# Performance work log

Hardware: AMD Instinct MI355X
Metric: run time of the kernel (lower is better)

Reference implementation:

```python
import jax, jax.numpy as jnp
import numpy as np

N = 50000      # nodes
E = 800000     # edges
F = 128        # input features
H = 128        # hidden dim
G = 1024       # graphs in batch
EPS = 1e-5


def setup_inputs() -> dict:
    key = jax.random.key(0)
    ks = jax.random.split(key, 16)
    s = 0.05
    return {
        "x": jax.random.normal(ks[0], (N, F), dtype=jnp.float32),
        "edge_index": jax.random.randint(ks[1], (2, E), 0, N, dtype=jnp.int64),
        "batch": jnp.sort(jax.random.randint(ks[2], (N,), 0, G, dtype=jnp.int64)),
        "convW0": jax.random.normal(ks[3], (F, H), dtype=jnp.float32) * s,
        "convW": jax.random.normal(ks[4], (2, H, H), dtype=jnp.float32) * s,  # layers 1,2
        "convb": jax.random.normal(ks[5], (3, H), dtype=jnp.float32) * s,
        "bn_gamma": jnp.ones((3, H), dtype=jnp.float32),
        "bn_beta": jnp.zeros((3, H), dtype=jnp.float32),
        "mW1": jax.random.normal(ks[6], (2 * H, 256), dtype=jnp.float32) * s,
        "mb1": jnp.zeros((256,), dtype=jnp.float32),
        "mW2": jax.random.normal(ks[7], (256, 128), dtype=jnp.float32) * s,
        "mb2": jnp.zeros((128,), dtype=jnp.float32),
        "mW3": jax.random.normal(ks[8], (128, 1), dtype=jnp.float32) * s,
        "mb3": jnp.zeros((1,), dtype=jnp.float32),
    }


def _gcn_norm(edge_index):
    # add self-loops, compute sym-normalization coeffs (PyG GCNConv default)
    loop = jnp.arange(N, dtype=edge_index.dtype)
    src = jnp.concatenate([edge_index[0], loop])
    dst = jnp.concatenate([edge_index[1], loop])
    deg = jax.ops.segment_sum(jnp.ones_like(dst, dtype=jnp.float32), dst, num_segments=N)
    dinv = jax.lax.rsqrt(deg)  # deg >= 1 due to self loops
    norm = dinv[src] * dinv[dst]  # [E+N]
    return src, dst, norm


def _gcn_layer(x, W, b, src, dst, norm):
    h = x @ W                               # [N, H]
    msg = h[src] * norm[:, None]            # gather + scale, [E+N, H]
    agg = jax.ops.segment_sum(msg, dst, num_segments=N)
    return agg + b


def _batchnorm(x, gamma, beta):
    mu = jnp.mean(x, axis=0)
    var = jnp.mean(jnp.square(x - mu), axis=0)  # biased, as torch training fwd
    return gamma * (x - mu) * jax.lax.rsqrt(var + EPS) + beta


def reference(x, edge_index, batch, convW0, convW, convb, bn_gamma, bn_beta,
              mW1, mb1, mW2, mb2, mW3, mb3):
    src, dst, norm = _gcn_norm(edge_index)
    Ws = [convW0, convW[0], convW[1]]
    for i in range(3):
        x = _gcn_layer(x, Ws[i], convb[i], src, dst, norm)
        x = _batchnorm(x, bn_gamma[i], bn_beta[i])
        x = jax.nn.relu(x)
        # dropout: identity in eval mode
    ones = jnp.ones((N,), dtype=x.dtype)
    counts = jax.ops.segment_sum(ones, batch, num_segments=G)  # [G]
    x_mean = jax.ops.segment_sum(x, batch, num_segments=G) / jnp.maximum(counts, 1.0)[:, None]
    x_max = jax.ops.segment_max(x, batch, num_segments=G)
    x_max = jnp.where(counts[:, None] > 0, x_max, 0.0)
    g = jnp.concatenate([x_mean, x_max], axis=1)  # [G, 2H]
    h = jax.nn.relu(g @ mW1 + mb1)
    h = jax.nn.relu(h @ mW2 + mb2)
    out = h @ mW3 + mb3                            # [G, 1]
    return out.squeeze(1)
```

## Files before the change

### kernel.cpp

```cpp
#include <hip/hip_runtime.h>


constexpr int FH = 128;
constexpr int GG = 1024;
constexpr int NSB = 128;
constexpr int BKS = 1024;
constexpr int CPAD = 16;
constexpr int EPB = 4096;
constexpr float EPSV = 1e-5f;

typedef __attribute__((ext_vector_type(8))) short short8v;
typedef __attribute__((ext_vector_type(4))) float f32x4;

__device__ inline unsigned short bf16_rn(float x) {
    unsigned u = __float_as_uint(x);
    unsigned r = (u + 0x7FFFu + ((u >> 16) & 1u)) >> 16;
    return (unsigned short)r;
}
__device__ inline float bflo(unsigned u) { return __uint_as_float(u << 16); }
__device__ inline float bfhi(unsigned u) { return __uint_as_float(u & 0xFFFF0000u); }

__global__ void k_deg(const int* __restrict__ dst, unsigned* __restrict__ deg, int E) {
    int e = blockIdx.x * 256 + threadIdx.x;
    if (e < E) atomicAdd(&deg[dst[e]], 1u);
}

__global__ __launch_bounds__(1024) void k_scan1(const unsigned* __restrict__ deg,
                                                int* __restrict__ rowptr, int* __restrict__ bsum,
                                                float* __restrict__ dinv, int n) {
    __shared__ int wsum[16];
    int i = blockIdx.x * 1024 + threadIdx.x;
    int lane = threadIdx.x & 63, wid = threadIdx.x >> 6;
    int v = (i < n) ? (int)deg[i] : 0;
    if (i < n) dinv[i] = rsqrtf((float)v + 1.0f);
    int incl = v;
    #pragma unroll
    for (int off = 1; off < 64; off <<= 1) {
        int t = __shfl_up(incl, off, 64);
        if (lane >= off) incl += t;
    }
    if (lane == 63) wsum[wid] = incl;
    __syncthreads();
    int woff = 0;
    #pragma unroll
    for (int w = 0; w < 16; ++w) woff += (w < wid) ? wsum[w] : 0;
    if (i < n) rowptr[i] = woff + incl - v;
    if (threadIdx.x == 1023) bsum[blockIdx.x] = woff + incl;
}

__global__ void k_scan2(int* __restrict__ bsum, int* __restrict__ rowptr_n, int nb) {
    int lane = threadIdx.x;
    int v = (lane < nb) ? bsum[lane] : 0;
    int incl = v;
    #pragma unroll
    for (int off = 1; off < 64; off <<= 1) {
        int t = __shfl_up(incl, off, 64);
        if (lane >= off) incl += t;
    }
    if (lane < nb) bsum[lane] = incl - v;
    if (lane == 63) *rowptr_n = incl;
}

__global__ __launch_bounds__(1024) void k_scan3(int* __restrict__ rowptr,
                                                const int* __restrict__ bsum,
                                                int* __restrict__ bcur, int n) {
    int i = blockIdx.x * 1024 + threadIdx.x;
    if (i < n) {
        int r = rowptr[i] + bsum[blockIdx.x];
        rowptr[i] = r;
        if ((i & 63) == 0) bcur[(i >> 6) * CPAD] = r;
    }
}

__global__ __launch_bounds__(256) void k_binscatter(const int* __restrict__ src, const int* __restrict__ dst,
                                                    int* __restrict__ bcur, unsigned* __restrict__ tmp,
                                                    int E, int nbk) {
    __shared__ int hist[BKS];
    int tid = threadIdx.x;
    for (int b = tid; b < nbk; b += 256) hist[b] = 0;
    __syncthreads();
    int e0 = blockIdx.x * EPB;
    int s[16], d[16];
    #pragma unroll
    for (int i = 0; i < 16; ++i) {
        int e = e0 + i * 256 + tid;
        if (e < E) {
            s[i] = src[e]; d[i] = dst[e];
            atomicAdd(&hist[d[i] >> 6], 1);
        } else d[i] = -1;
    }
    __syncthreads();
    for (int b = tid; b < nbk; b += 256) {
        int c = hist[b];
        hist[b] = c ? atomicAdd(&bcur[b * CPAD], c) : 0;
    }
    __syncthreads();
    #pragma unroll
    for (int i = 0; i < 16; ++i) {
        if (d[i] >= 0) {
            int p = atomicAdd(&hist[d[i] >> 6], 1);
            tmp[p] = (unsigned)s[i] | ((unsigned)(d[i] & 63) << 16);
        }
    }
}

__global__ __launch_bounds__(256) void k_finesort(const unsigned* __restrict__ tmp,
                                                  const int* __restrict__ rowptr,
                                                  int* __restrict__ csr_src, int n) {
    __shared__ int cur[64];
    int nb0 = blockIdx.x << 6;
    int tid = threadIdx.x;
    int hi = min(nb0 + 64, n);
    if (tid < 64 && nb0 + tid < n) cur[tid] = rowptr[nb0 + tid];
    __syncthreads();
    int estart = rowptr[nb0], eend = rowptr[hi];
    for (int e = estart + tid; e < eend; e += 256) {
        unsigned pr = tmp[e];
        int p = atomicAdd(&cur[(pr >> 16) & 63], 1);
        csr_src[p] = (int)(pr & 0xFFFFu);
    }
}

__global__ void k_gptr(const int* __restrict__ batch, int* __restrict__ gptr, int n) {
    int g = blockIdx.x * 256 + threadIdx.x;
    if (g > GG) return;
    int lo = 0, hi = n;
    while (lo < hi) { int mid = (lo + hi) >> 1; if (batch[mid] < g) lo = mid + 1; else hi = mid; }
    gptr[g] = lo;
}

__global__ void k_wprep(const float* __restrict__ W0, const float* __restrict__ W12,
                        unsigned short* __restrict__ Wt) {
    int t = blockIdx.x * 256 + threadIdx.x;
    int l = t >> 14, o = t & 16383;
    const float* W = (l == 0) ? W0 : W12 + (size_t)(l - 1) * 16384;
    int j = o & 7, c = (o >> 3) & 15, hi = (o >> 7) & 3, kb = (o >> 9) & 3, nt = o >> 11;
    int k = kb * 32 + hi * 8 + j;
    int col = nt * 16 + c;
    Wt[t] = bf16_rn(W[k * 128 + col]);
}

template<bool BF16IN>
__global__ __launch_bounds__(256) void k_gemm(const void* __restrict__ Xp,
                                              const unsigned short* __restrict__ Wt,
                                              const float* __restrict__ dinv,
                                              const float* __restrict__ sc,
                                              const float* __restrict__ sh,
                                              unsigned short* __restrict__ H, int n) {
    int wave = threadIdx.x >> 6, L = threadIdx.x & 63;
    int hi = L >> 4, c16 = L & 15;
    int m0 = blockIdx.x * 64 + wave * 16;
    int arow = m0 + c16;
    bool okA = arow < n;

    short8v aF[4];
    #pragma unroll
    for (int kb = 0; kb < 4; ++kb) {
        int kc = kb * 32 + hi * 8;
        float v[8];
        #pragma unroll
        for (int j = 0; j < 8; ++j) v[j] = 0.f;
        if (okA) {
            if constexpr (BF16IN) {
                const unsigned short* Xb = (const unsigned short*)Xp;
                uint4 raw = *(const uint4*)&Xb[(size_t)arow * 128 + kc];
                v[0] = bflo(raw.x); v[1] = bfhi(raw.x);
                v[2] = bflo(raw.y); v[3] = bfhi(raw.y);
                v[4] = bflo(raw.z); v[5] = bfhi(raw.z);
                v[6] = bflo(raw.w); v[7] = bfhi(raw.w);
                float4 s0 = *(const float4*)&sc[kc], s1 = *(const float4*)&sc[kc + 4];
                float4 h0 = *(const float4*)&sh[kc], h1 = *(const float4*)&sh[kc + 4];
                v[0] = fmaxf(fmaf(v[0], s0.x, h0.x), 0.f);
                v[1] = fmaxf(fmaf(v[1], s0.y, h0.y), 0.f);
                v[2] = fmaxf(fmaf(v[2], s0.z, h0.z), 0.f);
                v[3] = fmaxf(fmaf(v[3], s0.w, h0.w), 0.f);
                v[4] = fmaxf(fmaf(v[4], s1.x, h1.x), 0.f);
                v[5] = fmaxf(fmaf(v[5], s1.y, h1.y), 0.f);
                v[6] = fmaxf(fmaf(v[6], s1.z, h1.z), 0.f);
                v[7] = fmaxf(fmaf(v[7], s1.w, h1.w), 0.f);
            } else {
                const float* Xf = (const float*)Xp;
                float4 v0 = *(const float4*)&Xf[(size_t)arow * 128 + kc];
                float4 v1 = *(const float4*)&Xf[(size_t)arow * 128 + kc + 4];
                v[0] = v0.x; v[1] = v0.y; v[2] = v0.z; v[3] = v0.w;
                v[4] = v1.x; v[5] = v1.y; v[6] = v1.z; v[7] = v1.w;
            }
        }
        short8v a;
        #pragma unroll
        for (int j = 0; j < 8; ++j) a[j] = (short)bf16_rn(v[j]);
        aF[kb] = a;
    }

    f32x4 acc[8];
    #pragma unroll
    for (int nt = 0; nt < 8; ++nt) {
        acc[nt][0] = 0.f; acc[nt][1] = 0.f; acc[nt][2] = 0.f; acc[nt][3] = 0.f;
    }
    #pragma unroll
    for (int nt = 0; nt < 8; ++nt) {
        #pragma unroll
        for (int kb = 0; kb < 4; ++kb) {
            short8v bF = *(const short8v*)&Wt[(size_t)(nt * 4 + kb) * 512 + L * 8];
            acc[nt] = __builtin_amdgcn_mfma_f32_16x16x32_bf16(aF[kb], bF, acc[nt], 0, 0, 0);
        }
    }

    #pragma unroll
    for (int reg = 0; reg < 4; ++reg) {
        int row = m0 + hi * 4 + reg;
        if (row < n) {
            float dv = dinv[row];
            #pragma unroll
            for (int nt = 0; nt < 8; ++nt)
                H[(size_t)row * 128 + nt * 16 + c16] = bf16_rn(acc[nt][reg] * dv);
        }
    }
}

__global__ __launch_bounds__(256) void k_aggregate(const int* __restrict__ rowptr, const int* __restrict__ csr_src,
                                                   const float* __restrict__ dinv,
                                                   const unsigned short* __restrict__ H2,
                                                   unsigned short* __restrict__ Bo, int n) {
    int node = blockIdx.x * 16 + (threadIdx.x >> 4);
    if (node >= n) return;
    int lane = threadIdx.x & 15;
    int beg = rowptr[node], end = rowptr[node + 1];
    float dv = dinv[node];
    const uint4* Hv = (const uint4*)H2;
    float a0[8], a1[8];
    {
        uint4 u = Hv[(size_t)node * 16 + lane];
        a0[0] = bflo(u.x); a0[1] = bfhi(u.x); a0[2] = bflo(u.y); a0[3] = bfhi(u.y);
        a0[4] = bflo(u.z); a0[5] = bfhi(u.z); a0[6] = bflo(u.w); a0[7] = bfhi(u.w);
        #pragma unroll
        for (int j = 0; j < 8; ++j) a1[j] = 0.f;
    }
    int e = beg;
    for (; e + 3 < end; e += 4) {
        int s0 = csr_src[e], s1 = csr_src[e + 1], s2 = csr_src[e + 2], s3 = csr_src[e + 3];
        uint4 u0 = Hv[(size_t)s0 * 16 + lane];
        uint4 u1 = Hv[(size_t)s1 * 16 + lane];
        uint4 u2 = Hv[(size_t)s2 * 16 + lane];
        uint4 u3 = Hv[(size_t)s3 * 16 + lane];
        a0[0] += bflo(u0.x); a0[1] += bfhi(u0.x); a0[2] += bflo(u0.y); a0[3] += bfhi(u0.y);
        a0[4] += bflo(u0.z); a0[5] += bfhi(u0.z); a0[6] += bflo(u0.w); a0[7] += bfhi(u0.w);
        a1[0] += bflo(u1.x); a1[1] += bfhi(u1.x); a1[2] += bflo(u1.y); a1[3] += bfhi(u1.y);
        a1[4] += bflo(u1.z); a1[5] += bfhi(u1.z); a1[6] += bflo(u1.w); a1[7] += bfhi(u1.w);
        a0[0] += bflo(u2.x); a0[1] += bfhi(u2.x); a0[2] += bflo(u2.y); a0[3] += bfhi(u2.y);
        a0[4] += bflo(u2.z); a0[5] += bfhi(u2.z); a0[6] += bflo(u2.w); a0[7] += bfhi(u2.w);
        a1[0] += bflo(u3.x); a1[1] += bfhi(u3.x); a1[2] += bflo(u3.y); a1[3] += bfhi(u3.y);
        a1[4] += bflo(u3.z); a1[5] += bfhi(u3.z); a1[6] += bflo(u3.w); a1[7] += bfhi(u3.w);
    }
    for (; e < end; ++e) {
        int s0 = csr_src[e];
        uint4 u0 = Hv[(size_t)s0 * 16 + lane];
        a0[0] += bflo(u0.x); a0[1] += bfhi(u0.x); a0[2] += bflo(u0.y); a0[3] += bfhi(u0.y);
        a0[4] += bflo(u0.z); a0[5] += bfhi(u0.z); a0[6] += bflo(u0.w); a0[7] += bfhi(u0.w);
    }
    unsigned w0 = (unsigned)bf16_rn((a0[0] + a1[0]) * dv) | ((unsigned)bf16_rn((a0[1] + a1[1]) * dv) << 16);
    unsigned w1 = (unsigned)bf16_rn((a0[2] + a1[2]) * dv) | ((unsigned)bf16_rn((a0[3] + a1[3]) * dv) << 16);
    unsigned w2 = (unsigned)bf16_rn((a0[4] + a1[4]) * dv) | ((unsigned)bf16_rn((a0[5] + a1[5]) * dv) << 16);
    unsigned w3 = (unsigned)bf16_rn((a0[6] + a1[6]) * dv) | ((unsigned)bf16_rn((a0[7] + a1[7]) * dv) << 16);
    ((uint4*)Bo)[(size_t)node * 16 + lane] = make_uint4(w0, w1, w2, w3);
}

__global__ __launch_bounds__(256) void k_stats(const unsigned short* __restrict__ X,
                                               float* __restrict__ partials, int n) {
    __shared__ float sb[4][128];
    int tid = threadIdx.x;
    int fp = tid & 63, sub = tid >> 6;
    float s0 = 0.f, s1 = 0.f, q0 = 0.f, q1 = 0.f;
    for (int r = blockIdx.x * 4 + sub; r < n; r += NSB * 4) {
        unsigned u = *(const unsigned*)&X[(size_t)r * 128 + fp * 2];
        float v0 = bflo(u), v1 = bfhi(u);
        s0 += v0; q0 = fmaf(v0, v0, q0);
        s1 += v1; q1 = fmaf(v1, v1, q1);
    }
    sb[sub][fp * 2] = s0; sb[sub][fp * 2 + 1] = s1;
    __syncthreads();
    if (tid < 128) partials[(size_t)blockIdx.x * 256 + tid] =
        sb[0][tid] + sb[1][tid] + sb[2][tid] + sb[3][tid];
    __syncthreads();
    sb[sub][fp * 2] = q0; sb[sub][fp * 2 + 1] = q1;
    __syncthreads();
    if (tid < 128) partials[(size_t)blockIdx.x * 256 + 128 + tid] =
        sb[0][tid] + sb[1][tid] + sb[2][tid] + sb[3][tid];
}

__global__ __launch_bounds__(256) void k_finstats(const float* __restrict__ partials,
                                                  const float* __restrict__ gamma, const float* __restrict__ beta,
                                                  float* __restrict__ sc, float* __restrict__ sh, int n) {
    __shared__ float red[256];
    int t = threadIdx.x;
    int f = t & 127, half = t >> 7;
    float s = 0.f, q = 0.f;
    for (int b = half * (NSB / 2); b < (half + 1) * (NSB / 2); ++b) {
        s += partials[(size_t)b * 256 + f];
        q += partials[(size_t)b * 256 + 128 + f];
    }
    red[t] = s;
    __syncthreads();
    float s_tot = red[f] + red[f + 128];
    __syncthreads();
    red[t] = q;
    __syncthreads();
    if (half == 0) {
        float q_tot = red[f] + red[f + 128];
        float invN = 1.0f / (float)n;
        float mu = s_tot * invN;
        float var = fmaf(-mu, mu, q_tot * invN);
        float scale = gamma[f] * rsqrtf(var + EPSV);
        sc[f] = scale;
        sh[f] = fmaf(-mu, scale, beta[f]);
    }
}

__global__ __launch_bounds__(256) void k_pool(const unsigned short* __restrict__ X, const int* __restrict__ gptr,
                                              const float* __restrict__ sc, const float* __restrict__ sh,
                                              float* __restrict__ pooled) {
    __shared__ float shm[256];
    int g = blockIdx.x;
    int t = threadIdx.x;
    int f = t & 127, sub = t >> 7;
    int beg = gptr[g], end = gptr[g + 1];
    float scf = sc[f], shf = sh[f];
    float s = 0.f, m = 0.f;
    for (int r = beg + sub; r < end; r += 2) {
        float xv = __uint_as_float((unsigned)X[(size_t)r * 128 + f] << 16);
        float v = fmaxf(fmaf(xv, scf, shf), 0.f);
        s += v; m = fmaxf(m, v);
    }
    shm[t] = s;
    __syncthreads();
    if (sub == 0) {
        int c = end - beg;
        float inv = (c > 0) ? 1.0f / (float)c : 0.f;
        pooled[(size_t)g * 256 + f] = (s + shm[t + 128]) * inv;
    }
    __syncthreads();
    shm[t] = m;
    __syncthreads();
    if (sub == 1) {
        pooled[(size_t)g * 256 + 128 + f] = fmaxf(m, shm[t - 128]);
    }
}

__global__ __launch_bounds__(256) void k_mlp1(const float* __restrict__ pooled, const float* __restrict__ W1,
                                              const float* __restrict__ b1, float* __restrict__ H1) {
    __shared__ float grow[256];
    int gi = blockIdx.x, t = threadIdx.x;
    grow[t] = pooled[(size_t)gi * 256 + t];
    __syncthreads();
    float acc = b1[t];
    #pragma unroll 8
    for (int k = 0; k < 256; ++k) acc = fmaf(grow[k], W1[k * 256 + t], acc);
    H1[gi * 256 + t] = fmaxf(acc, 0.f);
}

__global__ __launch_bounds__(128) void k_mlp23(const float* __restrict__ H1, const float* __restrict__ W2,
                                               const float* __restrict__ b2, const float* __restrict__ W3,
                                               const float* __restrict__ b3, float* __restrict__ out) {
    __shared__ float row[256];
    __shared__ float wred[2];
    int gi = blockIdx.x, t = threadIdx.x;
    row[t] = H1[gi * 256 + t];
    row[t + 128] = H1[gi * 256 + t + 128];
    __syncthreads();
    float acc = b2[t];
    #pragma unroll 8
    for (int k = 0; k < 256; ++k) acc = fmaf(row[k], W2[k * 128 + t], acc);
    float v = fmaxf(acc, 0.f) * W3[t];
    #pragma unroll
    for (int off = 32; off; off >>= 1) v += __shfl_down(v, off);
    if ((t & 63) == 0) wred[t >> 6] = v;
    __syncthreads();
    if (t == 0) out[gi] = wred[0] + wred[1] + b3[0];
}

extern "C" void kernel_launch(void* const* d_in, const int* in_sizes, int n_in,
                              void* d_out, int out_size, void* d_ws, size_t ws_size,
                              hipStream_t stream) {
    const float* x      = (const float*)d_in[0];
    const int*   ei     = (const int*)d_in[1];
    const int*   batch  = (const int*)d_in[2];
    const float* convW0 = (const float*)d_in[3];
    const float* convW  = (const float*)d_in[4];
    const float* gamma  = (const float*)d_in[6];
    const float* beta   = (const float*)d_in[7];
    const float* mW1    = (const float*)d_in[8];
    const float* mb1    = (const float*)d_in[9];
    const float* mW2    = (const float*)d_in[10];
    const float* mb2    = (const float*)d_in[11];
    const float* mW3    = (const float*)d_in[12];
    const float* mb3    = (const float*)d_in[13];
    float* out = (float*)d_out;

    const int E = in_sizes[1] / 2;
    const int n = in_sizes[0] / FH;
    const int npad = (n + 4) & ~3;
    const int nb = (n + 1023) / 1024;
    const int nbk = (n + 63) >> 6;

    float*          A     = (float*)d_ws;
    unsigned short* H2b   = (unsigned short*)A;
    unsigned*       tmp   = (unsigned*)A;
    float*    B       = A + (size_t)n * FH;
    unsigned short* Bb = (unsigned short*)B;
    int*      bcur    = (int*)B;
    float*    dinv    = B + (size_t)n * FH;
    unsigned* deg     = (unsigned*)(dinv + n);
    float*    parts   = (float*)(deg + n);
    float*    sc      = parts + (size_t)NSB * 256;
    float*    sh      = sc + 128;
    float*    pooled  = sh + 128;
    float*    h1      = pooled + (size_t)GG * 256;
    int*      gptr    = (int*)(h1 + (size_t)GG * 256);
    int*      rowptr  = gptr + ((GG + 4) & ~3);
    int*      bsum    = rowptr + npad;
    int*      csrsrc  = bsum + 64;
    unsigned short* Wt = (unsigned short*)(csrsrc + ((E + 3) & ~3));

    const int* srcI = ei;
    const int* dstI = ei + E;

    hipMemsetAsync(deg, 0, (size_t)n * sizeof(unsigned), stream);
    k_deg<<<(E + 255) / 256, 256, 0, stream>>>(dstI, deg, E);
    k_scan1<<<nb, 1024, 0, stream>>>(deg, rowptr, bsum, dinv, n);
    k_scan2<<<1, 64, 0, stream>>>(bsum, rowptr + n, nb);
    k_scan3<<<nb, 1024, 0, stream>>>(rowptr, bsum, bcur, n);
    k_binscatter<<<(E + EPB - 1) / EPB, 256, 0, stream>>>(srcI, dstI, bcur, tmp, E, nbk);
    k_finesort<<<nbk, 256, 0, stream>>>(tmp, rowptr, csrsrc, n);
    k_gptr<<<(GG + 1 + 255) / 256, 256, 0, stream>>>(batch, gptr, n);
    k_wprep<<<3 * 16384 / 256, 256, 0, stream>>>(convW0, convW, Wt);

    for (int l = 0; l < 3; ++l) {
        if (l == 0)
            k_gemm<false><<<(n + 63) / 64, 256, 0, stream>>>(x, Wt, dinv, nullptr, nullptr, H2b, n);
        else
            k_gemm<true><<<(n + 63) / 64, 256, 0, stream>>>(Bb, Wt + (size_t)l * 16384, dinv, sc, sh, H2b, n);
        k_aggregate<<<(n + 15) / 16, 256, 0, stream>>>(rowptr, csrsrc, dinv, H2b, Bb, n);
        k_stats<<<NSB, 256, 0, stream>>>(Bb, parts, n);
        k_finstats<<<1, 256, 0, stream>>>(parts, gamma + l * FH, beta + l * FH, sc, sh, n);
    }

    k_pool<<<GG, 256, 0, stream>>>(Bb, gptr, sc, sh, pooled);
    k_mlp1<<<GG, 256, 0, stream>>>(pooled, mW1, mb1, h1);
    k_mlp23<<<GG, 128, 0, stream>>>(h1, mW2, mb2, mW3, mb3, out);
}
```

Baseline: 459.1 us.

## Fuse GCN aggregation with batchnorm statistics in a persistent grid-stride kernel

Merges the neighbor aggregation and the per-feature sum and sum-of-squares reduction into one kernel. Each 32-lane group handles one node at a time in a grid-stride loop over 512 blocks, so the separate stats pass that re-read the aggregated output is gone. Lanes now load 8 bytes instead of 16 and unroll the edge loop by 2 instead of 4, which lowers memory-level parallelism per lane. A fixed 512-block grid may also underuse the GPU compared with one block per 16 nodes. The finalization kernel is widened to 512 threads to reduce the larger set of partials.

```diff
diff --git a/kernel.cpp b/kernel.cpp
--- a/kernel.cpp
+++ b/kernel.cpp
@@ -3,7 +3,7 @@
 
 constexpr int FH = 128;
 constexpr int GG = 1024;
-constexpr int NSB = 128;
+constexpr int NAB = 512;
 constexpr int BKS = 1024;
 constexpr int CPAD = 16;
 constexpr int EPB = 4096;
@@ -19,6 +19,10 @@
 }
 __device__ inline float bflo(unsigned u) { return __uint_as_float(u << 16); }
 __device__ inline float bfhi(unsigned u) { return __uint_as_float(u & 0xFFFF0000u); }
+__device__ inline float bfs(unsigned short h) { return __uint_as_float((unsigned)h << 16); }
+__device__ inline float4 bf4tof(ushort4 h) {
+    return make_float4(bfs(h.x), bfs(h.y), bfs(h.z), bfs(h.w));
+}
 
 __global__ void k_deg(const int* __restrict__ dst, unsigned* __restrict__ deg, int E) {
     int e = blockIdx.x * 256 + threadIdx.x;
@@ -218,95 +222,80 @@
     }
 }
 
-__global__ __launch_bounds__(256) void k_aggregate(const int* __restrict__ rowptr, const int* __restrict__ csr_src,
-                                                   const float* __restrict__ dinv,
-                                                   const unsigned short* __restrict__ H2,
-                                                   unsigned short* __restrict__ Bo, int n) {
-    int node = blockIdx.x * 16 + (threadIdx.x >> 4);
-    if (node >= n) return;
-    int lane = threadIdx.x & 15;
-    int beg = rowptr[node], end = rowptr[node + 1];
-    float dv = dinv[node];
-    const uint4* Hv = (const uint4*)H2;
-    float a0[8], a1[8];
-    {
-        uint4 u = Hv[(size_t)node * 16 + lane];
-        a0[0] = bflo(u.x); a0[1] = bfhi(u.x); a0[2] = bflo(u.y); a0[3] = bfhi(u.y);
-        a0[4] = bflo(u.z); a0[5] = bfhi(u.z); a0[6] = bflo(u.w); a0[7] = bfhi(u.w);
-        #pragma unroll
-        for (int j = 0; j < 8; ++j) a1[j] = 0.f;
-    }
-    int e = beg;
-    for (; e + 3 < end; e += 4) {
-        int s0 = csr_src[e], s1 = csr_src[e + 1], s2 = csr_src[e + 2], s3 = csr_src[e + 3];
-        uint4 u0 = Hv[(size_t)s0 * 16 + lane];
-        uint4 u1 = Hv[(size_t)s1 * 16 + lane];
-        uint4 u2 = Hv[(size_t)s2 * 16 + lane];
-        uint4 u3 = Hv[(size_t)s3 * 16 + lane];
-        a0[0] += bflo(u0.x); a0[1] += bfhi(u0.x); a0[2] += bflo(u0.y); a0[3] += bfhi(u0.y);
-        a0[4] += bflo(u0.z); a0[5] += bfhi(u0.z); a0[6] += bflo(u0.w); a0[7] += bfhi(u0.w);
-        a1[0] += bflo(u1.x); a1[1] += bfhi(u1.x); a1[2] += bflo(u1.y); a1[3] += bfhi(u1.y);
-        a1[4] += bflo(u1.z); a1[5] += bfhi(u1.z); a1[6] += bflo(u1.w); a1[7] += bfhi(u1.w);
-        a0[0] += bflo(u2.x); a0[1] += bfhi(u2.x); a0[2] += bflo(u2.y); a0[3] += bfhi(u2.y);
-        a0[4] += bflo(u2.z); a0[5] += bfhi(u2.z); a0[6] += bflo(u2.w); a0[7] += bfhi(u2.w);
-        a1[0] += bflo(u3.x); a1[1] += bfhi(u3.x); a1[2] += bflo(u3.y); a1[3] += bfhi(u3.y);
-        a1[4] += bflo(u3.z); a1[5] += bfhi(u3.z); a1[6] += bflo(u3.w); a1[7] += bfhi(u3.w);
-    }
-    for (; e < end; ++e) {
-        int s0 = csr_src[e];
-        uint4 u0 = Hv[(size_t)s0 * 16 + lane];
-        a0[0] += bflo(u0.x); a0[1] += bfhi(u0.x); a0[2] += bflo(u0.y); a0[3] += bfhi(u0.y);
-        a0[4] += bflo(u0.z); a0[5] += bfhi(u0.z); a0[6] += bflo(u0.w); a0[7] += bfhi(u0.w);
-    }
-    unsigned w0 = (unsigned)bf16_rn((a0[0] + a1[0]) * dv) | ((unsigned)bf16_rn((a0[1] + a1[1]) * dv) << 16);
-    unsigned w1 = (unsigned)bf16_rn((a0[2] + a1[2]) * dv) | ((unsigned)bf16_rn((a0[3] + a1[3]) * dv) << 16);
-    unsigned w2 = (unsigned)bf16_rn((a0[4] + a1[4]) * dv) | ((unsigned)bf16_rn((a0[5] + a1[5]) * dv) << 16);
-    unsigned w3 = (unsigned)bf16_rn((a0[6] + a1[6]) * dv) | ((unsigned)bf16_rn((a0[7] + a1[7]) * dv) << 16);
-    ((uint4*)Bo)[(size_t)node * 16 + lane] = make_uint4(w0, w1, w2, w3);
-}
-
-__global__ __launch_bounds__(256) void k_stats(const unsigned short* __restrict__ X,
-                                               float* __restrict__ partials, int n) {
-    __shared__ float sb[4][128];
+__global__ __launch_bounds__(256) void k_aggstats(const int* __restrict__ rowptr, const int* __restrict__ csr_src,
+                                                  const float* __restrict__ dinv,
+                                                  const unsigned short* __restrict__ H2,
+                                                  unsigned short* __restrict__ Bo,
+                                                  float* __restrict__ partials, int n) {
+    __shared__ float sb[8][128];
     int tid = threadIdx.x;
-    int fp = tid & 63, sub = tid >> 6;
-    float s0 = 0.f, s1 = 0.f, q0 = 0.f, q1 = 0.f;
-    for (int r = blockIdx.x * 4 + sub; r < n; r += NSB * 4) {
-        unsigned u = *(const unsigned*)&X[(size_t)r * 128 + fp * 2];
-        float v0 = bflo(u), v1 = bfhi(u);
-        s0 += v0; q0 = fmaf(v0, v0, q0);
-        s1 += v1; q1 = fmaf(v1, v1, q1);
-    }
-    sb[sub][fp * 2] = s0; sb[sub][fp * 2 + 1] = s1;
+    int sub = tid >> 5, lane = tid & 31;
+    const ushort4* Hv = (const ushort4*)H2;
+    float sA[4] = {0.f, 0.f, 0.f, 0.f}, qA[4] = {0.f, 0.f, 0.f, 0.f};
+    for (int node = blockIdx.x * 8 + sub; node < n; node += NAB * 8) {
+        int beg = rowptr[node], end = rowptr[node + 1];
+        float dv = dinv[node];
+        float4 acc = bf4tof(Hv[(size_t)node * 32 + lane]);
+        float4 acc2 = make_float4(0.f, 0.f, 0.f, 0.f);
+        int e = beg;
+        for (; e + 1 < end; e += 2) {
+            int s0 = csr_src[e], s1 = csr_src[e + 1];
+            float4 h0 = bf4tof(Hv[(size_t)s0 * 32 + lane]);
+            float4 h1 = bf4tof(Hv[(size_t)s1 * 32 + lane]);
+            acc.x += h0.x;  acc.y += h0.y;  acc.z += h0.z;  acc.w += h0.w;
+            acc2.x += h1.x; acc2.y += h1.y; acc2.z += h1.z; acc2.w += h1.w;
+        }
+        if (e < end) {
+            int s0 = csr_src[e];
+            float4 h0 = bf4tof(Hv[(size_t)s0 * 32 + lane]);
+            acc.x += h0.x; acc.y += h0.y; acc.z += h0.z; acc.w += h0.w;
+        }
+        ushort4 o;
+        o.x = bf16_rn((acc.x + acc2.x) * dv);
+        o.y = bf16_rn((acc.y + acc2.y) * dv);
+        o.z = bf16_rn((acc.z + acc2.z) * dv);
+        o.w = bf16_rn((acc.w + acc2.w) * dv);
+        *(ushort4*)&Bo[(size_t)node * 128 + lane * 4] = o;
+        float v0 = bfs(o.x), v1 = bfs(o.y), v2 = bfs(o.z), v3 = bfs(o.w);
+        sA[0] += v0; qA[0] = fmaf(v0, v0, qA[0]);
+        sA[1] += v1; qA[1] = fmaf(v1, v1, qA[1]);
+        sA[2] += v2; qA[2] = fmaf(v2, v2, qA[2]);
+        sA[3] += v3; qA[3] = fmaf(v3, v3, qA[3]);
+    }
+    #pragma unroll
+    for (int j = 0; j < 4; ++j) sb[sub][lane * 4 + j] = sA[j];
     __syncthreads();
     if (tid < 128) partials[(size_t)blockIdx.x * 256 + tid] =
-        sb[0][tid] + sb[1][tid] + sb[2][tid] + sb[3][tid];
-    __syncthreads();
-    sb[sub][fp * 2] = q0; sb[sub][fp * 2 + 1] = q1;
+        sb[0][tid] + sb[1][tid] + sb[2][tid] + sb[3][tid] +
+        sb[4][tid] + sb[5][tid] + sb[6][tid] + sb[7][tid];
+    __syncthreads();
+    #pragma unroll
+    for (int j = 0; j < 4; ++j) sb[sub][lane * 4 + j] = qA[j];
     __syncthreads();
     if (tid < 128) partials[(size_t)blockIdx.x * 256 + 128 + tid] =
-        sb[0][tid] + sb[1][tid] + sb[2][tid] + sb[3][tid];
-}
-
-__global__ __launch_bounds__(256) void k_finstats(const float* __restrict__ partials,
+        sb[0][tid] + sb[1][tid] + sb[2][tid] + sb[3][tid] +
+        sb[4][tid] + sb[5][tid] + sb[6][tid] + sb[7][tid];
+}
+
+__global__ __launch_bounds__(512) void k_finstats(const float* __restrict__ partials,
                                                   const float* __restrict__ gamma, const float* __restrict__ beta,
                                                   float* __restrict__ sc, float* __restrict__ sh, int n) {
-    __shared__ float red[256];
+    __shared__ float red[512];
     int t = threadIdx.x;
-    int f = t & 127, half = t >> 7;
+    int f = t & 127, q4 = t >> 7;
     float s = 0.f, q = 0.f;
-    for (int b = half * (NSB / 2); b < (half + 1) * (NSB / 2); ++b) {
+    for (int b = q4 * (NAB / 4); b < (q4 + 1) * (NAB / 4); ++b) {
         s += partials[(size_t)b * 256 + f];
         q += partials[(size_t)b * 256 + 128 + f];
     }
     red[t] = s;
     __syncthreads();
-    float s_tot = red[f] + red[f + 128];
+    float s_tot = red[f] + red[f + 128] + red[f + 256] + red[f + 384];
     __syncthreads();
     red[t] = q;
     __syncthreads();
-    if (half == 0) {
-        float q_tot = red[f] + red[f + 128];
+    if (q4 == 0) {
+        float q_tot = red[f] + red[f + 128] + red[f + 256] + red[f + 384];
         float invN = 1.0f / (float)n;
         float mu = s_tot * invN;
         float var = fmaf(-mu, mu, q_tot * invN);
@@ -327,7 +316,7 @@
     float scf = sc[f], shf = sh[f];
     float s = 0.f, m = 0.f;
     for (int r = beg + sub; r < end; r += 2) {
-        float xv = __uint_as_float((unsigned)X[(size_t)r * 128 + f] << 16);
+        float xv = bfs(X[(size_t)r * 128 + f]);
         float v = fmaxf(fmaf(xv, scf, shf), 0.f);
         s += v; m = fmaxf(m, v);
     }
@@ -411,7 +400,7 @@
     float*    dinv    = B + (size_t)n * FH;
     unsigned* deg     = (unsigned*)(dinv + n);
     float*    parts   = (float*)(deg + n);
-    float*    sc      = parts + (size_t)NSB * 256;
+    float*    sc      = parts + (size_t)NAB * 256;
     float*    sh      = sc + 128;
     float*    pooled  = sh + 128;
     float*    h1      = pooled + (size_t)GG * 256;
@@ -439,9 +428,8 @@
             k_gemm<false><<<(n + 63) / 64, 256, 0, stream>>>(x, Wt, dinv, nullptr, nullptr, H2b, n);
         else
             k_gemm<true><<<(n + 63) / 64, 256, 0, stream>>>(Bb, Wt + (size_t)l * 16384, dinv, sc, sh, H2b, n);
-        k_aggregate<<<(n + 15) / 16, 256, 0, stream>>>(rowptr, csrsrc, dinv, H2b, Bb, n);
-        k_stats<<<NSB, 256, 0, stream>>>(Bb, parts, n);
-        k_finstats<<<1, 256, 0, stream>>>(parts, gamma + l * FH, beta + l * FH, sc, sh, n);
+        k_aggstats<<<NAB, 256, 0, stream>>>(rowptr, csrsrc, dinv, H2b, Bb, parts, n);
+        k_finstats<<<1, 512, 0, stream>>>(parts, gamma + l * FH, beta + l * FH, sc, sh, n);
     }
 
     k_pool<<<GG, 256, 0, stream>>>(Bb, gptr, sc, sh, pooled);
```

Measured after the change: 627.4 us. 1.37x slower.
